# Kernel tuning notes

Hardware: AMD Instinct MI355X
Metric: run time of the kernel (lower is better)

## Reference

```python
import jax, jax.numpy as jnp
import numpy as np

EPS = 1e-5

def grid_sample_bilinear(img, grid):
    """torch F.grid_sample, mode='bilinear', padding_mode='zeros', align_corners=True.
    img: (b, c, H, W); grid: (b, Hg, Wg, 2) with (x, y) in [-1, 1]. Returns (b, c, Hg, Wg)."""
    H, W = img.shape[2], img.shape[3]
    x = (grid[..., 0] + 1.0) * 0.5 * (W - 1)
    y = (grid[..., 1] + 1.0) * 0.5 * (H - 1)
    x0 = jnp.floor(x); y0 = jnp.floor(y)
    x1 = x0 + 1.0;     y1 = y0 + 1.0
    wx1 = x - x0; wx0 = 1.0 - wx1
    wy1 = y - y0; wy0 = 1.0 - wy1

    def sample_one(img_b, yi, xi):
        # img_b: (c,H,W); yi, xi: (Hg,Wg) float corner coords
        valid = ((yi >= 0) & (yi < H) & (xi >= 0) & (xi < W)).astype(img_b.dtype)
        yc = jnp.clip(yi, 0, H - 1).astype(jnp.int32)
        xc = jnp.clip(xi, 0, W - 1).astype(jnp.int32)
        return img_b[:, yc, xc] * valid[None]  # (c,Hg,Wg)

    def per_batch(img_b, x0b, x1b, y0b, y1b, wx0b, wx1b, wy0b, wy1b):
        v = (sample_one(img_b, y0b, x0b) * (wy0b * wx0b)[None]
             + sample_one(img_b, y0b, x1b) * (wy0b * wx1b)[None]
             + sample_one(img_b, y1b, x0b) * (wy1b * wx0b)[None]
             + sample_one(img_b, y1b, x1b) * (wy1b * wx1b)[None])
        return v

    return jax.vmap(per_batch)(img, x0, x1, y0, y1, wx0, wx1, wy0, wy1)


def conv_bn_relu(x, w, gamma, beta):
    # 1x1 conv (no bias) + BatchNorm2d (batch stats, training-mode forward) + ReLU
    y = jnp.einsum('nchw,oc->nohw', x, w)
    mean = y.mean(axis=(0, 2, 3), keepdims=True)
    var = y.var(axis=(0, 2, 3), keepdims=True)
    y = (y - mean) * jax.lax.rsqrt(var + EPS)
    y = y * gamma[None, :, None, None] + beta[None, :, None, None]
    return jax.nn.relu(y)


def setup_inputs() -> dict:
    key = jax.random.key(0)
    ks = jax.random.split(key, 10)
    b, c, h, w, r = 1, 128, 64, 128, 4
    d = 2 * r + 1
    f1 = jax.random.normal(ks[0], (b, c, h, w), dtype=jnp.float32)
    f2 = jax.random.normal(ks[1], (b, c, h, w), dtype=jnp.float32)
    # coords: base pixel grid (x, y) plus a small random flow perturbation
    gy, gx = jnp.meshgrid(jnp.arange(h, dtype=jnp.float32), jnp.arange(w, dtype=jnp.float32), indexing='ij')
    base = jnp.stack([gx, gy], axis=0)[None]  # (1,2,h,w)
    coords = base + 2.0 * jax.random.normal(ks[2], (b, 2, h, w), dtype=jnp.float32)
    c1, c2, c3 = 96, 128, 64
    w1 = jax.random.normal(ks[3], (c1, 2 * c), dtype=jnp.float32) * 0.05
    w2 = jax.random.normal(ks[4], (c2, c1), dtype=jnp.float32) * 0.05
    w3 = jax.random.normal(ks[5], (c3, c2), dtype=jnp.float32) * 0.05
    w4 = jax.random.normal(ks[6], (1, c3), dtype=jnp.float32) * 0.05
    b4 = jnp.zeros((1,), dtype=jnp.float32)
    g1 = jnp.ones((c1,), jnp.float32); be1 = jnp.zeros((c1,), jnp.float32)
    g2 = jnp.ones((c2,), jnp.float32); be2 = jnp.zeros((c2,), jnp.float32)
    g3 = jnp.ones((c3,), jnp.float32); be3 = jnp.zeros((c3,), jnp.float32)
    # DAP: identity init + small noise so gradients are non-trivial
    wdap = jnp.eye(d * d, dtype=jnp.float32) + 0.01 * jax.random.normal(ks[7], (d * d, d * d), dtype=jnp.float32)
    return {"f1": f1, "f2": f2, "coords": coords,
            "w1": w1, "g1": g1, "be1": be1,
            "w2": w2, "g2": g2, "be2": be2,
            "w3": w3, "g3": g3, "be3": be3,
            "w4": w4, "b4": b4, "wdap": wdap, "radius": 4}


def reference(f1, f2, coords, w1, g1, be1, w2, g2, be2, w3, g3, be3, w4, b4, wdap, radius):
    b, c, h, w = f1.shape
    r = radius
    d = 2 * r + 1
    dx = jnp.linspace(-r, r, d, dtype=f1.dtype)
    delta = jnp.stack(jnp.meshgrid(dx, dx, indexing='ij'), axis=-1)  # (d,d,2)
    coords_p = jnp.transpose(coords, (0, 2, 3, 1))  # (b,h,w,2)
    cent = coords_p[:, None, :, None, :, :] + delta.reshape(1, d, 1, d, 1, 2)  # (b,d,h,d,w,2)
    cx = 2.0 * cent[..., 0] / (w - 1) - 1.0
    cy = 2.0 * cent[..., 1] / (h - 1) - 1.0
    grid = jnp.stack([cx, cy], axis=-1).reshape(b, d * h, d * w, 2)
    f2s = grid_sample_bilinear(f2, grid)                     # (b,c,d*h,d*w)
    f2s = f2s.reshape(b, c, d, h, d, w).transpose(0, 2, 4, 1, 3, 5)  # (b,d,d,c,h,w)
    f1e = jnp.broadcast_to(f1[:, None, None], (b, d, d, c, h, w))
    corr = jnp.concatenate([f1e, f2s], axis=3).reshape(b * d * d, 2 * c, h, w)
    x = conv_bn_relu(corr, w1, g1, be1)
    x = conv_bn_relu(x, w2, g2, be2)
    x = conv_bn_relu(x, w3, g3, be3)
    cost = jnp.einsum('nchw,oc->nohw', x, w4) + b4[None, :, None, None]  # (b*d*d,1,h,w)
    cost = cost.reshape(b, d * d, h, w)
    # DAP: 1x1 conv over the d*d displacement channels, no bias
    cost = jnp.einsum('bkhw,lk->blhw', cost, wdap)
    return cost  # (b, (2r+1)^2, h, w)
```

## Files before the change

### kernel.cpp

```cpp
#include <hip/hip_runtime.h>
#include <hip/hip_bf16.h>

#define H 64
#define W 128
#define P 8192
#define DD 81
#define NS 663552
#define C1 96
#define C2 128
#define C3 64
#define EPSF 1e-5f
#define NSLOT 128

#define X1S 104
#define X2S 136
#define X1TS 136

#define NGB 324
#define NGSLOT 8

typedef __attribute__((ext_vector_type(8))) short bf16x8;
typedef __attribute__((ext_vector_type(4))) float f32x4;

#define S1SUM 0
#define S1SSQ (S1SUM + NSLOT * C1)
#define M1SUM (S1SSQ + NSLOT * C1)
#define S3SUM (M1SUM + NSLOT * C1)
#define S3SSQ (S3SUM + NSLOT * C3)
#define GSLOT (S3SSQ + NSLOT * C3)
#define STATS_ZERO_FLOATS (GSLOT + NGSLOT * 9216)
#define S1Sc 126976
#define S1Tc (S1Sc + C1)
#define S2Sc (S1Tc + C1)
#define S2Tc (S2Sc + C2)
#define S3Sc (S2Tc + C2)
#define S3Tc (S3Sc + C3)
#define GOFF 127552
#define COST_OFF (GOFF + 9216)
#define FLOAT_END (COST_OFF + NS)
#define A_BYTE   ((size_t)FLOAT_END * 4)
#define G_BYTE   (A_BYTE + (size_t)P * 96 * 2)
#define W2BF_BYTE (G_BYTE + (size_t)P * 96 * 2)
#define W3BF_BYTE (W2BF_BYTE + (size_t)C2 * C1 * 2)
#define Y1_BYTE  (W3BF_BYTE + (size_t)C3 * C2 * 2)
#define Y3_BYTE  (Y1_BYTE + (size_t)NS * C1 * 2)
#define WS_NEEDED (Y3_BYTE + (size_t)NS * C3 * 2)

__device__ __forceinline__ float bflo(unsigned u) { return __uint_as_float(u << 16); }
__device__ __forceinline__ float bfhi(unsigned u) { return __uint_as_float(u & 0xffff0000u); }
__device__ __forceinline__ float bfu(unsigned short v) { return __uint_as_float((unsigned)v << 16); }

__device__ __forceinline__ unsigned pkbf(float a, float b) {
  __hip_bfloat162 h = __float22bfloat162_rn(make_float2(a, b));
  unsigned u; __builtin_memcpy(&u, &h, 4);
  return u;
}

__global__ __launch_bounds__(256) void k_prep(const float* __restrict__ f1,
                                              const float* __restrict__ f2,
                                              const float* __restrict__ w1,
                                              unsigned short* __restrict__ aT,
                                              unsigned short* __restrict__ gT) {
  __shared__ float tile[128][64];
  int t = threadIdx.x;
  int p0 = blockIdx.x * 64;
  int px = t & 63, q = t >> 6;
  int c0 = q * 24;
  for (int pass = 0; pass < 2; ++pass) {
    const float* src = pass ? f2 : f1;
    unsigned short* dst = pass ? gT : aT;
    int koff = pass ? 128 : 0;
    __syncthreads();
    for (int idx = t; idx < 8192; idx += 256) {
      int kk = idx >> 6, xx = idx & 63;
      tile[kk][xx] = src[kk * P + p0 + xx];
    }
    __syncthreads();
    float acc[24];
#pragma unroll
    for (int i = 0; i < 24; ++i) acc[i] = 0.f;
    for (int kk = 0; kk < 128; ++kk) {
      float fv = tile[kk][px];
#pragma unroll
      for (int i = 0; i < 24; ++i)
        acc[i] += w1[(c0 + i) * 256 + koff + kk] * fv;
    }
#pragma unroll
    for (int i = 0; i < 24; i += 4) {
      uint2 pk;
      pk.x = pkbf(acc[i + 0], acc[i + 1]);
      pk.y = pkbf(acc[i + 2], acc[i + 3]);
      *(uint2*)(dst + ((size_t)((c0 + i) >> 2) * P + p0 + px) * 4) = pk;
    }
  }
}

__global__ void k_wprep(const float* __restrict__ w2, const float* __restrict__ w3,
                        unsigned short* __restrict__ w2bf, unsigned short* __restrict__ w3bf) {
  int idx = blockIdx.x * 256 + threadIdx.x;
  if (idx < C2 * C1) {
    w2bf[idx] = (unsigned short)(pkbf(w2[idx], 0.f) & 0xffffu);
  } else if (idx < C2 * C1 + C3 * C2) {
    w3bf[idx - C2 * C1] = (unsigned short)(pkbf(w3[idx - C2 * C1], 0.f) & 0xffffu);
  }
}

__global__ __launch_bounds__(256) void k_sample(const float* __restrict__ coords,
                                                float* __restrict__ ws,
                                                const unsigned short* __restrict__ aT,
                                                const unsigned short* __restrict__ gT,
                                                unsigned short* __restrict__ y1T) {
  int t = threadIdx.x, b = blockIdx.x;
  int sub = b % 12;
  int ptile = b / 12;
  int cg = sub >> 1, jh = sub & 1;
  int j0 = jh * 5;
  int nj = 5 - jh;
  int c = cg * 4 + (t >> 6);
  int px = t & 63;
  int p = ptile * 64 + px;
  float cx = coords[p], cy = coords[P + p];
  float fx0 = floorf(cx), fy0 = floorf(cy);
  float wx1 = cx - fx0, wx0 = 1.f - wx1;
  float wy1 = cy - fy0, wy0 = 1.f - wy1;
  int ixb = (int)fx0 - 4 + j0, iyb = (int)fy0 - 4;
  int colOff[6];
  float vxv[6];
#pragma unroll
  for (int j = 0; j < 6; ++j) {
    int ix = ixb + j;
    vxv[j] = (ix >= 0 && ix < W) ? 1.f : 0.f;
    colOff[j] = min(max(ix, 0), W - 1);
  }
  float ewx0[5], ewx1[5];
#pragma unroll
  for (int j = 0; j < 5; ++j) { ewx0[j] = wx0 * vxv[j]; ewx1[j] = wx1 * vxv[j + 1]; }
  float av[4];
  {
    uint2 a2 = *(const uint2*)(aT + ((size_t)c * P + p) * 4);
    av[0] = bflo(a2.x); av[1] = bfhi(a2.x); av[2] = bflo(a2.y); av[3] = bfhi(a2.y);
  }
  const unsigned short* gc = gT + (size_t)c * P * 4;
  unsigned short* yb = y1T + ((size_t)c * P + p) * 4;
  float Hb[2][5][4];
  float sum[4] = {0.f, 0.f, 0.f, 0.f}, ssq[4] = {0.f, 0.f, 0.f, 0.f};
  float vyPrev = 0.f;
#pragma unroll
  for (int dy = 0; dy < 10; ++dy) {
    const int cur = dy & 1, prv = cur ^ 1;
    int iy = iyb + dy;
    float vy = (iy >= 0 && iy < H) ? 1.f : 0.f;
    const unsigned short* grow = gc + (size_t)(min(max(iy, 0), H - 1) * W) * 4;
    uint2 gv[6];
#pragma unroll
    for (int j = 0; j < 6; ++j) gv[j] = *(const uint2*)(grow + colOff[j] * 4);
#pragma unroll
    for (int j = 0; j < 5; ++j) {
      Hb[cur][j][0] = fmaf(ewx1[j], bflo(gv[j + 1].x), ewx0[j] * bflo(gv[j].x));
      Hb[cur][j][1] = fmaf(ewx1[j], bfhi(gv[j + 1].x), ewx0[j] * bfhi(gv[j].x));
      Hb[cur][j][2] = fmaf(ewx1[j], bflo(gv[j + 1].y), ewx0[j] * bflo(gv[j].y));
      Hb[cur][j][3] = fmaf(ewx1[j], bfhi(gv[j + 1].y), ewx0[j] * bfhi(gv[j].y));
    }
    if (dy >= 1) {
      const int dyk = dy - 1;
      float e0 = wy0 * vyPrev, e1 = wy1 * vy;
#pragma unroll
      for (int j = 0; j < 5; ++j) {
        if (j < nj) {
          float o0 = fmaf(e0, Hb[prv][j][0], fmaf(e1, Hb[cur][j][0], av[0]));
          float o1 = fmaf(e0, Hb[prv][j][1], fmaf(e1, Hb[cur][j][1], av[1]));
          float o2 = fmaf(e0, Hb[prv][j][2], fmaf(e1, Hb[cur][j][2], av[2]));
          float o3 = fmaf(e0, Hb[prv][j][3], fmaf(e1, Hb[cur][j][3], av[3]));
          sum[0] += o0; ssq[0] = fmaf(o0, o0, ssq[0]);
          sum[1] += o1; ssq[1] = fmaf(o1, o1, ssq[1]);
          sum[2] += o2; ssq[2] = fmaf(o2, o2, ssq[2]);
          sum[3] += o3; ssq[3] = fmaf(o3, o3, ssq[3]);
          uint2 pk;
          pk.x = pkbf(o0, o1);
          pk.y = pkbf(o2, o3);
          int kk = (j0 + j) * 9 + dyk;
          *(uint2*)(yb + (size_t)kk * 24 * P * 4) = pk;
        }
      }
    }
    vyPrev = vy;
  }
#pragma unroll
  for (int m = 1; m < 64; m <<= 1) {
#pragma unroll
    for (int e = 0; e < 4; ++e) {
      sum[e] += __shfl_xor(sum[e], m);
      ssq[e] += __shfl_xor(ssq[e], m);
    }
  }
  if ((t & 63) == 0) {
    int slot = b & (NSLOT - 1);
#pragma unroll
    for (int e = 0; e < 4; ++e) {
      atomicAdd(&ws[S1SUM + slot * C1 + c * 4 + e], sum[e]);
      atomicAdd(&ws[S1SSQ + slot * C1 + c * 4 + e], ssq[e]);
    }
  }
}

__global__ void k_finalize(float* __restrict__ ws, int sumO, int ssqO,
                           const float* __restrict__ gamma, const float* __restrict__ beta,
                           int sO, int tO, int C) {
  int c = threadIdx.x;
  if (c < C) {
    float su = 0.f, sq = 0.f;
    for (int s = 0; s < NSLOT; ++s) { su += ws[sumO + s * C + c]; sq += ws[ssqO + s * C + c]; }
    float mean = su * (1.0f / (float)NS);
    float var = sq * (1.0f / (float)NS) - mean * mean;
    float sc = gamma[c] * rsqrtf(var + EPSF);
    ws[sO + c] = sc;
    ws[tO + c] = beta[c] - mean * sc;
  }
}

__global__ __launch_bounds__(256) void k_gram(const unsigned short* __restrict__ y1T,
                                              float* __restrict__ ws) {
  __shared__ unsigned short x1t[96 * X1TS];
  int t = threadIdx.x, b = blockIdx.x;
  int w = t >> 6, l = t & 63;
  int lr = l & 15, lh = l >> 4;
  int i0 = (w >> 1) * 48, j0 = (w & 1) * 48;
  f32x4 acc[9];
  f32x4 zero4 = {0.f, 0.f, 0.f, 0.f};
#pragma unroll
  for (int q = 0; q < 9; ++q) acc[q] = zero4;
  int c = t >> 3, pg = t & 7;
  float s1v[4], t1v[4];
  if (c < 24) {
#pragma unroll
    for (int e = 0; e < 4; ++e) { s1v[e] = ws[S1Sc + c * 4 + e]; t1v[e] = ws[S1Tc + c * 4 + e]; }
  }
  float msum[4] = {0.f, 0.f, 0.f, 0.f};
  for (int it = 0; it < 16; ++it) {
    int idx = b * 16 + it;
    int k = idx >> 6, p0 = (idx & 63) << 7;
    const unsigned short* y1k = y1T + (size_t)k * P * 96;
    __syncthreads();
    if (c < 24) {
      int pbase = p0 + pg * 16;
      unsigned rowu[4][8];
#pragma unroll
      for (int ii = 0; ii < 8; ++ii) {
        uint4 v = *(const uint4*)(y1k + ((size_t)c * P + pbase + ii * 2) * 4);
        float x00 = fmaxf(0.f, fmaf(s1v[0], bflo(v.x), t1v[0]));
        float x10 = fmaxf(0.f, fmaf(s1v[1], bfhi(v.x), t1v[1]));
        float x20 = fmaxf(0.f, fmaf(s1v[2], bflo(v.y), t1v[2]));
        float x30 = fmaxf(0.f, fmaf(s1v[3], bfhi(v.y), t1v[3]));
        float x01 = fmaxf(0.f, fmaf(s1v[0], bflo(v.z), t1v[0]));
        float x11 = fmaxf(0.f, fmaf(s1v[1], bfhi(v.z), t1v[1]));
        float x21 = fmaxf(0.f, fmaf(s1v[2], bflo(v.w), t1v[2]));
        float x31 = fmaxf(0.f, fmaf(s1v[3], bfhi(v.w), t1v[3]));
        msum[0] += x00 + x01; msum[1] += x10 + x11;
        msum[2] += x20 + x21; msum[3] += x30 + x31;
        rowu[0][ii] = pkbf(x00, x01);
        rowu[1][ii] = pkbf(x10, x11);
        rowu[2][ii] = pkbf(x20, x21);
        rowu[3][ii] = pkbf(x30, x31);
      }
#pragma unroll
      for (int e = 0; e < 4; ++e) {
        unsigned short* dst = x1t + (c * 4 + e) * X1TS + pg * 16;
        uint4 pk0; pk0.x = rowu[e][0]; pk0.y = rowu[e][1]; pk0.z = rowu[e][2]; pk0.w = rowu[e][3];
        uint4 pk1; pk1.x = rowu[e][4]; pk1.y = rowu[e][5]; pk1.z = rowu[e][6]; pk1.w = rowu[e][7];
        *(uint4*)dst = pk0;
        *(uint4*)(dst + 8) = pk1;
      }
    }
    __syncthreads();
#pragma unroll
    for (int kk = 0; kk < 4; ++kk) {
      bf16x8 a3[3], b3[3];
#pragma unroll
      for (int a = 0; a < 3; ++a)
        a3[a] = *(const bf16x8*)(const void*)(x1t + (i0 + a * 16 + lr) * X1TS + kk * 32 + lh * 8);
#pragma unroll
      for (int bb = 0; bb < 3; ++bb)
        b3[bb] = *(const bf16x8*)(const void*)(x1t + (j0 + bb * 16 + lr) * X1TS + kk * 32 + lh * 8);
#pragma unroll
      for (int a = 0; a < 3; ++a)
#pragma unroll
        for (int bb = 0; bb < 3; ++bb)
          acc[a * 3 + bb] = __builtin_amdgcn_mfma_f32_16x16x32_bf16(a3[a], b3[bb], acc[a * 3 + bb], 0, 0, 0);
    }
  }
  {
    float* gp = ws + GSLOT + (b & (NGSLOT - 1)) * 9216;
#pragma unroll
    for (int a = 0; a < 3; ++a)
#pragma unroll
      for (int bb = 0; bb < 3; ++bb) {
        int ti = (w >> 1) * 3 + a, tj = (w & 1) * 3 + bb;
        f32x4 v = acc[a * 3 + bb];
#pragma unroll
        for (int r = 0; r < 4; ++r)
          atomicAdd(&gp[(ti * 16 + lh * 4 + r) * 96 + tj * 16 + lr], v[r]);
      }
  }
  if (c < 24) {
#pragma unroll
    for (int m = 1; m < 8; m <<= 1)
#pragma unroll
      for (int e = 0; e < 4; ++e) msum[e] += __shfl_xor(msum[e], m);
    if (pg == 0) {
      int slot = b & (NSLOT - 1);
#pragma unroll
      for (int e = 0; e < 4; ++e) atomicAdd(&ws[M1SUM + slot * C1 + c * 4 + e], msum[e]);
    }
  }
}

__global__ void k_greduce(float* __restrict__ ws) {
  int e = blockIdx.x * 256 + threadIdx.x;
  float s = 0.f;
#pragma unroll
  for (int g = 0; g < NGSLOT; ++g) s += ws[GSLOT + g * 9216 + e];
  ws[GOFF + e] = s;
}

__global__ __launch_bounds__(256) void k_fin2g(float* __restrict__ ws,
                                               const unsigned short* __restrict__ w2bf,
                                               const float* __restrict__ g2,
                                               const float* __restrict__ be2) {
  __shared__ float wrow[96];
  __shared__ float m1f[96];
  __shared__ float red[8];
  int o = blockIdx.x, t = threadIdx.x;
  if (t < 96) {
    wrow[t] = bfu(w2bf[o * 96 + t]);
    float s = 0.f;
    for (int sl = 0; sl < NSLOT; ++sl) s += ws[M1SUM + sl * C1 + t];
    m1f[t] = s;
  }
  __syncthreads();
  float quad = 0.f;
  for (int e = t; e < 9216; e += 256) {
    int i = e / 96, j = e - i * 96;
    quad = fmaf(wrow[i] * wrow[j], ws[GOFF + e], quad);
  }
  float msm = (t < 96) ? wrow[t] * m1f[t] : 0.f;
#pragma unroll
  for (int m = 1; m < 64; m <<= 1) { quad += __shfl_xor(quad, m); msm += __shfl_xor(msm, m); }
  if ((t & 63) == 0) { red[t >> 6] = quad; red[4 + (t >> 6)] = msm; }
  __syncthreads();
  if (t == 0) {
    float q = red[0] + red[1] + red[2] + red[3];
    float mm = red[4] + red[5] + red[6] + red[7];
    float mean = mm * (1.0f / (float)NS);
    float var = q * (1.0f / (float)NS) - mean * mean;
    float sc = g2[o] * rsqrtf(var + EPSF);
    ws[S2Sc + o] = sc;
    ws[S2Tc + o] = be2[o] - mean * sc;
  }
}

__device__ __forceinline__ void build_x1(const unsigned short* __restrict__ y1k,
                                         const float* __restrict__ ws,
                                         unsigned short* lds, int p0, int t) {
  int s = t >> 1, hh = t & 1;
  int p = p0 + s;
  const float* s1p = ws + S1Sc;
  const float* t1p = ws + S1Tc;
  unsigned short* base = lds + s * X1S + hh * 48;
#pragma unroll
  for (int i2 = 0; i2 < 6; ++i2) {
    int c0 = hh * 12 + i2 * 2;
    uint2 va = *(const uint2*)(y1k + ((size_t)c0 * P + p) * 4);
    uint2 vb = *(const uint2*)(y1k + ((size_t)(c0 + 1) * P + p) * 4);
    int cb = c0 * 4;
    float x0 = fmaxf(0.f, fmaf(s1p[cb + 0], bflo(va.x), t1p[cb + 0]));
    float x1 = fmaxf(0.f, fmaf(s1p[cb + 1], bfhi(va.x), t1p[cb + 1]));
    float x2 = fmaxf(0.f, fmaf(s1p[cb + 2], bflo(va.y), t1p[cb + 2]));
    float x3 = fmaxf(0.f, fmaf(s1p[cb + 3], bfhi(va.y), t1p[cb + 3]));
    float x4 = fmaxf(0.f, fmaf(s1p[cb + 4], bflo(vb.x), t1p[cb + 4]));
    float x5 = fmaxf(0.f, fmaf(s1p[cb + 5], bfhi(vb.x), t1p[cb + 5]));
    float x6 = fmaxf(0.f, fmaf(s1p[cb + 6], bflo(vb.y), t1p[cb + 6]));
    float x7 = fmaxf(0.f, fmaf(s1p[cb + 7], bfhi(vb.y), t1p[cb + 7]));
    uint4 pk;
    pk.x = pkbf(x0, x1); pk.y = pkbf(x2, x3); pk.z = pkbf(x4, x5); pk.w = pkbf(x6, x7);
    *(uint4*)(base + i2 * 8) = pk;
  }
}

__global__ __launch_bounds__(256) void k_l23(const unsigned short* __restrict__ y1T,
                                             float* __restrict__ ws,
                                             const unsigned short* __restrict__ w2bf,
                                             const unsigned short* __restrict__ w3bf,
                                             unsigned short* __restrict__ y3T) {
  __shared__ unsigned short ldss[128 * X1S];
  int t = threadIdx.x, b = blockIdx.x;
  int k = b >> 6, p0 = (b & 63) << 7;
  size_t n0 = (size_t)k * P + p0;
  int slot = b & (NSLOT - 1);
  const unsigned short* y1k = y1T + (size_t)k * P * 96;
  build_x1(y1k, ws, ldss, p0, t);
  __syncthreads();
  int l = t & 63, wv = t >> 6;
  int o0w = wv * 32;
  int lr = l & 15, lh = l >> 4;
  bf16x8 af[2][3];
#pragma unroll
  for (int m = 0; m < 2; ++m)
#pragma unroll
    for (int kk = 0; kk < 3; ++kk)
      af[m][kk] = *(const bf16x8*)(const void*)(w2bf + (size_t)(o0w + m * 16 + lr) * 96 + kk * 32 + lh * 8);
  f32x4 acc[2][8];
  f32x4 zero4 = {0.f, 0.f, 0.f, 0.f};
#pragma unroll
  for (int m = 0; m < 2; ++m)
#pragma unroll
    for (int n = 0; n < 8; ++n) acc[m][n] = zero4;
#pragma unroll
  for (int kk = 0; kk < 3; ++kk)
#pragma unroll
    for (int n = 0; n < 8; ++n) {
      bf16x8 bfr = *(const bf16x8*)(const void*)(ldss + (n * 16 + lr) * X1S + kk * 32 + lh * 8);
      acc[0][n] = __builtin_amdgcn_mfma_f32_16x16x32_bf16(af[0][kk], bfr, acc[0][n], 0, 0, 0);
      acc[1][n] = __builtin_amdgcn_mfma_f32_16x16x32_bf16(af[1][kk], bfr, acc[1][n], 0, 0, 0);
    }
  float s2v[2][4], t2v[2][4];
#pragma unroll
  for (int m = 0; m < 2; ++m)
#pragma unroll
    for (int r = 0; r < 4; ++r) {
      int cc = o0w + m * 16 + lh * 4 + r;
      s2v[m][r] = ws[S2Sc + cc];
      t2v[m][r] = ws[S2Tc + cc];
    }
  int o2 = wv * 16;
  int ch4 = wv * 4 + lh;
  bf16x8 af2[4];
#pragma unroll
  for (int kk = 0; kk < 4; ++kk)
    af2[kk] = *(const bf16x8*)(const void*)(w3bf + (size_t)(o2 + lr) * 128 + kk * 32 + lh * 8);
  unsigned short* x2s = ldss;
  float ssum[4] = {0.f, 0.f, 0.f, 0.f}, sssq[4] = {0.f, 0.f, 0.f, 0.f};
#pragma unroll
  for (int h = 0; h < 2; ++h) {
    __syncthreads();
#pragma unroll
    for (int m = 0; m < 2; ++m)
#pragma unroll
      for (int n2 = 0; n2 < 4; ++n2) {
        f32x4 v = acc[m][h * 4 + n2];
        float x0 = fmaxf(0.f, fmaf(s2v[m][0], v[0], t2v[m][0]));
        float x1v = fmaxf(0.f, fmaf(s2v[m][1], v[1], t2v[m][1]));
        float x2v = fmaxf(0.f, fmaf(s2v[m][2], v[2], t2v[m][2]));
        float x3 = fmaxf(0.f, fmaf(s2v[m][3], v[3], t2v[m][3]));
        uint2 pk;
        pk.x = pkbf(x0, x1v);
        pk.y = pkbf(x2v, x3);
        *(uint2*)(x2s + (n2 * 16 + lr) * X2S + o0w + m * 16 + lh * 4) = pk;
      }
    __syncthreads();
    f32x4 acc2[4];
#pragma unroll
    for (int n2 = 0; n2 < 4; ++n2) acc2[n2] = zero4;
#pragma unroll
    for (int kk = 0; kk < 4; ++kk)
#pragma unroll
      for (int n2 = 0; n2 < 4; ++n2) {
        bf16x8 bfr = *(const bf16x8*)(const void*)(x2s + (n2 * 16 + lr) * X2S + kk * 32 + lh * 8);
        acc2[n2] = __builtin_amdgcn_mfma_f32_16x16x32_bf16(af2[kk], bfr, acc2[n2], 0, 0, 0);
      }
#pragma unroll
    for (int n2 = 0; n2 < 4; ++n2) {
      f32x4 v = acc2[n2];
#pragma unroll
      for (int r = 0; r < 4; ++r) { float x = v[r]; ssum[r] += x; sssq[r] = fmaf(x, x, sssq[r]); }
      uint2 pk;
      pk.x = pkbf(v[0], v[1]);
      pk.y = pkbf(v[2], v[3]);
      size_t n = n0 + h * 64 + n2 * 16 + lr;
      *(uint2*)(y3T + ((size_t)ch4 * NS + n) * 4) = pk;
    }
  }
#pragma unroll
  for (int msk = 1; msk < 16; msk <<= 1)
#pragma unroll
    for (int i = 0; i < 4; ++i) { ssum[i] += __shfl_xor(ssum[i], msk); sssq[i] += __shfl_xor(sssq[i], msk); }
  if (lr == 0) {
#pragma unroll
    for (int r = 0; r < 4; ++r) {
      int o = o2 + lh * 4 + r;
      atomicAdd(&ws[S3SUM + slot * C3 + o], ssum[r]);
      atomicAdd(&ws[S3SSQ + slot * C3 + o], sssq[r]);
    }
  }
}

__global__ __launch_bounds__(256) void k_layer4(const unsigned short* __restrict__ y3T,
                                                float* __restrict__ ws,
                                                const float* __restrict__ w4,
                                                const float* __restrict__ b4) {
  size_t n = (size_t)blockIdx.x * 256 + threadIdx.x;
  const float* s3p = ws + S3Sc;
  const float* t3p = ws + S3Tc;
  float acc = 0.f;
#pragma unroll
  for (int c16 = 0; c16 < 16; ++c16) {
    uint2 v = *(const uint2*)(y3T + ((size_t)c16 * NS + n) * 4);
    int c = c16 * 4;
    acc += fmaxf(0.f, fmaf(s3p[c + 0], bflo(v.x), t3p[c + 0])) * w4[c + 0];
    acc += fmaxf(0.f, fmaf(s3p[c + 1], bfhi(v.x), t3p[c + 1])) * w4[c + 1];
    acc += fmaxf(0.f, fmaf(s3p[c + 2], bflo(v.y), t3p[c + 2])) * w4[c + 2];
    acc += fmaxf(0.f, fmaf(s3p[c + 3], bfhi(v.y), t3p[c + 3])) * w4[c + 3];
  }
  ws[COST_OFF + n] = acc + b4[0];
}

__global__ __launch_bounds__(256) void k_dap(const float* __restrict__ ws,
                                             const float* __restrict__ wdap,
                                             float* __restrict__ out) {
  __shared__ float wd[DD * DD];
  int t = threadIdx.x;
  for (int i = t; i < DD * DD; i += 256) wd[i] = wdap[i];
  __syncthreads();
  int p = blockIdx.x * 32 + (t & 31);
  int lg = t >> 5;
  const float* cost = ws + COST_OFF;
  float cr[81];
#pragma unroll
  for (int kk = 0; kk < 81; ++kk) cr[kk] = cost[kk * P + p];
  for (int l = lg; l < 81; l += 8) {
    float acc = 0.f;
#pragma unroll
    for (int kk = 0; kk < 81; ++kk) acc = fmaf(wd[l * 81 + kk], cr[kk], acc);
    out[(size_t)l * P + p] = acc;
  }
}

__global__ void k_marker(float* out) { out[0] = 1.0e30f; }

extern "C" void kernel_launch(void* const* d_in, const int* in_sizes, int n_in,
                              void* d_out, int out_size, void* d_ws, size_t ws_size,
                              hipStream_t stream) {
  const float* f1 = (const float*)d_in[0];
  const float* f2 = (const float*)d_in[1];
  const float* coords = (const float*)d_in[2];
  const float* w1 = (const float*)d_in[3];
  const float* g1 = (const float*)d_in[4];
  const float* be1 = (const float*)d_in[5];
  const float* w2 = (const float*)d_in[6];
  const float* g2 = (const float*)d_in[7];
  const float* be2 = (const float*)d_in[8];
  const float* w3 = (const float*)d_in[9];
  const float* g3 = (const float*)d_in[10];
  const float* be3 = (const float*)d_in[11];
  const float* w4 = (const float*)d_in[12];
  const float* b4 = (const float*)d_in[13];
  const float* wdap = (const float*)d_in[14];
  float* out = (float*)d_out;
  float* ws = (float*)d_ws;

  if (ws_size < WS_NEEDED) {
    k_marker<<<1, 1, 0, stream>>>(out);
    return;
  }
  unsigned short* aT = (unsigned short*)((char*)d_ws + A_BYTE);
  unsigned short* gT = (unsigned short*)((char*)d_ws + G_BYTE);
  unsigned short* w2bf = (unsigned short*)((char*)d_ws + W2BF_BYTE);
  unsigned short* w3bf = (unsigned short*)((char*)d_ws + W3BF_BYTE);
  unsigned short* y1T = (unsigned short*)((char*)d_ws + Y1_BYTE);
  unsigned short* y3T = (unsigned short*)((char*)d_ws + Y3_BYTE);

  hipMemsetAsync(d_ws, 0, (size_t)STATS_ZERO_FLOATS * 4, stream);
  k_prep<<<128, 256, 0, stream>>>(f1, f2, w1, aT, gT);
  k_wprep<<<80, 256, 0, stream>>>(w2, w3, w2bf, w3bf);
  k_sample<<<1536, 256, 0, stream>>>(coords, ws, aT, gT, y1T);
  k_finalize<<<1, 128, 0, stream>>>(ws, S1SUM, S1SSQ, g1, be1, S1Sc, S1Tc, C1);
  k_gram<<<NGB, 256, 0, stream>>>(y1T, ws);
  k_greduce<<<36, 256, 0, stream>>>(ws);
  k_fin2g<<<128, 256, 0, stream>>>(ws, w2bf, g2, be2);
  k_l23<<<5184, 256, 0, stream>>>(y1T, ws, w2bf, w3bf, y3T);
  k_finalize<<<1, 128, 0, stream>>>(ws, S3SUM, S3SSQ, g3, be3, S3Sc, S3Tc, C3);
  k_layer4<<<2592, 256, 0, stream>>>(y3T, ws, w4, b4);
  k_dap<<<256, 256, 0, stream>>>(ws, wdap, out);
}
```

Baseline: 284.9 us.

## Fuse layer-4 projection into DAP kernel and halve l23 tile per block

Merges the layer-4 1x1 conv (BN+ReLU+dot with w4) into the DAP kernel, so per-pixel cost values stay in shared memory instead of being written to and re-read from a global cost buffer, and one launch is removed. The l23 kernel now handles 64 pixels per block instead of 128 and launches twice as many blocks. That uses fewer accumulator registers and less LDS per block, which can raise occupancy, but the weight fragments are loaded more often. The fused kernel runs on only 256 blocks, so the layer-4 pass over y3T is spread across fewer blocks than before, which risks reduced parallelism.

```diff
diff --git a/kernel.cpp b/kernel.cpp
--- a/kernel.cpp
+++ b/kernel.cpp
@@ -36,8 +36,7 @@
 #define S3Sc (S2Tc + C2)
 #define S3Tc (S3Sc + C3)
 #define GOFF 127552
-#define COST_OFF (GOFF + 9216)
-#define FLOAT_END (COST_OFF + NS)
+#define FLOAT_END (GOFF + 9216)
 #define A_BYTE   ((size_t)FLOAT_END * 4)
 #define G_BYTE   (A_BYTE + (size_t)P * 96 * 2)
 #define W2BF_BYTE (G_BYTE + (size_t)P * 96 * 2)
@@ -358,46 +357,36 @@
   }
 }
 
-__device__ __forceinline__ void build_x1(const unsigned short* __restrict__ y1k,
-                                         const float* __restrict__ ws,
-                                         unsigned short* lds, int p0, int t) {
-  int s = t >> 1, hh = t & 1;
-  int p = p0 + s;
-  const float* s1p = ws + S1Sc;
-  const float* t1p = ws + S1Tc;
-  unsigned short* base = lds + s * X1S + hh * 48;
-#pragma unroll
-  for (int i2 = 0; i2 < 6; ++i2) {
-    int c0 = hh * 12 + i2 * 2;
-    uint2 va = *(const uint2*)(y1k + ((size_t)c0 * P + p) * 4);
-    uint2 vb = *(const uint2*)(y1k + ((size_t)(c0 + 1) * P + p) * 4);
-    int cb = c0 * 4;
-    float x0 = fmaxf(0.f, fmaf(s1p[cb + 0], bflo(va.x), t1p[cb + 0]));
-    float x1 = fmaxf(0.f, fmaf(s1p[cb + 1], bfhi(va.x), t1p[cb + 1]));
-    float x2 = fmaxf(0.f, fmaf(s1p[cb + 2], bflo(va.y), t1p[cb + 2]));
-    float x3 = fmaxf(0.f, fmaf(s1p[cb + 3], bfhi(va.y), t1p[cb + 3]));
-    float x4 = fmaxf(0.f, fmaf(s1p[cb + 4], bflo(vb.x), t1p[cb + 4]));
-    float x5 = fmaxf(0.f, fmaf(s1p[cb + 5], bfhi(vb.x), t1p[cb + 5]));
-    float x6 = fmaxf(0.f, fmaf(s1p[cb + 6], bflo(vb.y), t1p[cb + 6]));
-    float x7 = fmaxf(0.f, fmaf(s1p[cb + 7], bfhi(vb.y), t1p[cb + 7]));
-    uint4 pk;
-    pk.x = pkbf(x0, x1); pk.y = pkbf(x2, x3); pk.z = pkbf(x4, x5); pk.w = pkbf(x6, x7);
-    *(uint4*)(base + i2 * 8) = pk;
-  }
-}
-
 __global__ __launch_bounds__(256) void k_l23(const unsigned short* __restrict__ y1T,
                                              float* __restrict__ ws,
                                              const unsigned short* __restrict__ w2bf,
                                              const unsigned short* __restrict__ w3bf,
                                              unsigned short* __restrict__ y3T) {
-  __shared__ unsigned short ldss[128 * X1S];
+  __shared__ unsigned short ldss[64 * X2S];
   int t = threadIdx.x, b = blockIdx.x;
-  int k = b >> 6, p0 = (b & 63) << 7;
+  int k = b >> 7, p0 = (b & 127) << 6;
   size_t n0 = (size_t)k * P + p0;
   int slot = b & (NSLOT - 1);
   const unsigned short* y1k = y1T + (size_t)k * P * 96;
-  build_x1(y1k, ws, ldss, p0, t);
+  {
+    int s = t >> 2, q = t & 3;
+    int p = p0 + s;
+    const float* s1p = ws + S1Sc;
+    const float* t1p = ws + S1Tc;
+    unsigned short* base = ldss + s * X1S + q * 24;
+#pragma unroll
+    for (int i = 0; i < 6; ++i) {
+      int c4i = q * 6 + i;
+      uint2 v = *(const uint2*)(y1k + ((size_t)c4i * P + p) * 4);
+      int cb = c4i * 4;
+      float x0 = fmaxf(0.f, fmaf(s1p[cb + 0], bflo(v.x), t1p[cb + 0]));
+      float x1 = fmaxf(0.f, fmaf(s1p[cb + 1], bfhi(v.x), t1p[cb + 1]));
+      float x2 = fmaxf(0.f, fmaf(s1p[cb + 2], bflo(v.y), t1p[cb + 2]));
+      float x3 = fmaxf(0.f, fmaf(s1p[cb + 3], bfhi(v.y), t1p[cb + 3]));
+      uint2 pk; pk.x = pkbf(x0, x1); pk.y = pkbf(x2, x3);
+      *(uint2*)(base + i * 4) = pk;
+    }
+  }
   __syncthreads();
   int l = t & 63, wv = t >> 6;
   int o0w = wv * 32;
@@ -408,16 +397,16 @@
 #pragma unroll
     for (int kk = 0; kk < 3; ++kk)
       af[m][kk] = *(const bf16x8*)(const void*)(w2bf + (size_t)(o0w + m * 16 + lr) * 96 + kk * 32 + lh * 8);
-  f32x4 acc[2][8];
+  f32x4 acc[2][4];
   f32x4 zero4 = {0.f, 0.f, 0.f, 0.f};
 #pragma unroll
   for (int m = 0; m < 2; ++m)
 #pragma unroll
-    for (int n = 0; n < 8; ++n) acc[m][n] = zero4;
+    for (int n = 0; n < 4; ++n) acc[m][n] = zero4;
 #pragma unroll
   for (int kk = 0; kk < 3; ++kk)
 #pragma unroll
-    for (int n = 0; n < 8; ++n) {
+    for (int n = 0; n < 4; ++n) {
       bf16x8 bfr = *(const bf16x8*)(const void*)(ldss + (n * 16 + lr) * X1S + kk * 32 + lh * 8);
       acc[0][n] = __builtin_amdgcn_mfma_f32_16x16x32_bf16(af[0][kk], bfr, acc[0][n], 0, 0, 0);
       acc[1][n] = __builtin_amdgcn_mfma_f32_16x16x32_bf16(af[1][kk], bfr, acc[1][n], 0, 0, 0);
@@ -437,47 +426,43 @@
 #pragma unroll
   for (int kk = 0; kk < 4; ++kk)
     af2[kk] = *(const bf16x8*)(const void*)(w3bf + (size_t)(o2 + lr) * 128 + kk * 32 + lh * 8);
-  unsigned short* x2s = ldss;
+  __syncthreads();
+#pragma unroll
+  for (int m = 0; m < 2; ++m)
+#pragma unroll
+    for (int n2 = 0; n2 < 4; ++n2) {
+      f32x4 v = acc[m][n2];
+      float x0 = fmaxf(0.f, fmaf(s2v[m][0], v[0], t2v[m][0]));
+      float x1v = fmaxf(0.f, fmaf(s2v[m][1], v[1], t2v[m][1]));
+      float x2v = fmaxf(0.f, fmaf(s2v[m][2], v[2], t2v[m][2]));
+      float x3 = fmaxf(0.f, fmaf(s2v[m][3], v[3], t2v[m][3]));
+      uint2 pk;
+      pk.x = pkbf(x0, x1v);
+      pk.y = pkbf(x2v, x3);
+      *(uint2*)(ldss + (n2 * 16 + lr) * X2S + o0w + m * 16 + lh * 4) = pk;
+    }
+  __syncthreads();
+  f32x4 acc2[4];
+#pragma unroll
+  for (int n2 = 0; n2 < 4; ++n2) acc2[n2] = zero4;
+#pragma unroll
+  for (int kk = 0; kk < 4; ++kk)
+#pragma unroll
+    for (int n2 = 0; n2 < 4; ++n2) {
+      bf16x8 bfr = *(const bf16x8*)(const void*)(ldss + (n2 * 16 + lr) * X2S + kk * 32 + lh * 8);
+      acc2[n2] = __builtin_amdgcn_mfma_f32_16x16x32_bf16(af2[kk], bfr, acc2[n2], 0, 0, 0);
+    }
   float ssum[4] = {0.f, 0.f, 0.f, 0.f}, sssq[4] = {0.f, 0.f, 0.f, 0.f};
 #pragma unroll
-  for (int h = 0; h < 2; ++h) {
-    __syncthreads();
-#pragma unroll
-    for (int m = 0; m < 2; ++m)
-#pragma unroll
-      for (int n2 = 0; n2 < 4; ++n2) {
-        f32x4 v = acc[m][h * 4 + n2];
-        float x0 = fmaxf(0.f, fmaf(s2v[m][0], v[0], t2v[m][0]));
-        float x1v = fmaxf(0.f, fmaf(s2v[m][1], v[1], t2v[m][1]));
-        float x2v = fmaxf(0.f, fmaf(s2v[m][2], v[2], t2v[m][2]));
-        float x3 = fmaxf(0.f, fmaf(s2v[m][3], v[3], t2v[m][3]));
-        uint2 pk;
-        pk.x = pkbf(x0, x1v);
-        pk.y = pkbf(x2v, x3);
-        *(uint2*)(x2s + (n2 * 16 + lr) * X2S + o0w + m * 16 + lh * 4) = pk;
-      }
-    __syncthreads();
-    f32x4 acc2[4];
-#pragma unroll
-    for (int n2 = 0; n2 < 4; ++n2) acc2[n2] = zero4;
-#pragma unroll
-    for (int kk = 0; kk < 4; ++kk)
-#pragma unroll
-      for (int n2 = 0; n2 < 4; ++n2) {
-        bf16x8 bfr = *(const bf16x8*)(const void*)(x2s + (n2 * 16 + lr) * X2S + kk * 32 + lh * 8);
-        acc2[n2] = __builtin_amdgcn_mfma_f32_16x16x32_bf16(af2[kk], bfr, acc2[n2], 0, 0, 0);
-      }
-#pragma unroll
-    for (int n2 = 0; n2 < 4; ++n2) {
-      f32x4 v = acc2[n2];
-#pragma unroll
-      for (int r = 0; r < 4; ++r) { float x = v[r]; ssum[r] += x; sssq[r] = fmaf(x, x, sssq[r]); }
-      uint2 pk;
-      pk.x = pkbf(v[0], v[1]);
-      pk.y = pkbf(v[2], v[3]);
-      size_t n = n0 + h * 64 + n2 * 16 + lr;
-      *(uint2*)(y3T + ((size_t)ch4 * NS + n) * 4) = pk;
-    }
+  for (int n2 = 0; n2 < 4; ++n2) {
+    f32x4 v = acc2[n2];
+#pragma unroll
+    for (int r = 0; r < 4; ++r) { float x = v[r]; ssum[r] += x; sssq[r] = fmaf(x, x, sssq[r]); }
+    uint2 pk;
+    pk.x = pkbf(v[0], v[1]);
+    pk.y = pkbf(v[2], v[3]);
+    size_t n = n0 + n2 * 16 + lr;
+    *(uint2*)(y3T + ((size_t)ch4 * NS + n) * 4) = pk;
   }
 #pragma unroll
   for (int msk = 1; msk < 16; msk <<= 1)
@@ -493,44 +478,49 @@
   }
 }
 
-__global__ __launch_bounds__(256) void k_layer4(const unsigned short* __restrict__ y3T,
-                                                float* __restrict__ ws,
-                                                const float* __restrict__ w4,
-                                                const float* __restrict__ b4) {
-  size_t n = (size_t)blockIdx.x * 256 + threadIdx.x;
-  const float* s3p = ws + S3Sc;
-  const float* t3p = ws + S3Tc;
-  float acc = 0.f;
-#pragma unroll
-  for (int c16 = 0; c16 < 16; ++c16) {
-    uint2 v = *(const uint2*)(y3T + ((size_t)c16 * NS + n) * 4);
-    int c = c16 * 4;
-    acc += fmaxf(0.f, fmaf(s3p[c + 0], bflo(v.x), t3p[c + 0])) * w4[c + 0];
-    acc += fmaxf(0.f, fmaf(s3p[c + 1], bfhi(v.x), t3p[c + 1])) * w4[c + 1];
-    acc += fmaxf(0.f, fmaf(s3p[c + 2], bflo(v.y), t3p[c + 2])) * w4[c + 2];
-    acc += fmaxf(0.f, fmaf(s3p[c + 3], bfhi(v.y), t3p[c + 3])) * w4[c + 3];
-  }
-  ws[COST_OFF + n] = acc + b4[0];
-}
-
-__global__ __launch_bounds__(256) void k_dap(const float* __restrict__ ws,
-                                             const float* __restrict__ wdap,
-                                             float* __restrict__ out) {
+__global__ __launch_bounds__(256) void k_dap4(const unsigned short* __restrict__ y3T,
+                                              const float* __restrict__ ws,
+                                              const float* __restrict__ w4,
+                                              const float* __restrict__ b4,
+                                              const float* __restrict__ wdap,
+                                              float* __restrict__ out) {
   __shared__ float wd[DD * DD];
+  __shared__ float cs[DD][33];
+  __shared__ float coef[3][64];
   int t = threadIdx.x;
+  int p0 = blockIdx.x * 32;
   for (int i = t; i < DD * DD; i += 256) wd[i] = wdap[i];
-  __syncthreads();
-  int p = blockIdx.x * 32 + (t & 31);
-  int lg = t >> 5;
-  const float* cost = ws + COST_OFF;
-  float cr[81];
-#pragma unroll
-  for (int kk = 0; kk < 81; ++kk) cr[kk] = cost[kk * P + p];
-  for (int l = lg; l < 81; l += 8) {
+  if (t < 64) {
+    coef[0][t] = ws[S3Sc + t];
+    coef[1][t] = ws[S3Tc + t];
+    coef[2][t] = w4[t];
+  }
+  __syncthreads();
+  float b4v = b4[0];
+  int px = t & 31, kg = t >> 5;
+  for (int k = kg; k < DD; k += 8) {
+    size_t n = (size_t)k * P + p0 + px;
     float acc = 0.f;
 #pragma unroll
-    for (int kk = 0; kk < 81; ++kk) acc = fmaf(wd[l * 81 + kk], cr[kk], acc);
-    out[(size_t)l * P + p] = acc;
+    for (int c16 = 0; c16 < 16; ++c16) {
+      uint2 v = *(const uint2*)(y3T + ((size_t)c16 * NS + n) * 4);
+      int c = c16 * 4;
+      acc += fmaxf(0.f, fmaf(coef[0][c + 0], bflo(v.x), coef[1][c + 0])) * coef[2][c + 0];
+      acc += fmaxf(0.f, fmaf(coef[0][c + 1], bfhi(v.x), coef[1][c + 1])) * coef[2][c + 1];
+      acc += fmaxf(0.f, fmaf(coef[0][c + 2], bflo(v.y), coef[1][c + 2])) * coef[2][c + 2];
+      acc += fmaxf(0.f, fmaf(coef[0][c + 3], bfhi(v.y), coef[1][c + 3])) * coef[2][c + 3];
+    }
+    cs[k][px] = acc + b4v;
+  }
+  __syncthreads();
+  float cr[DD];
+#pragma unroll
+  for (int kk = 0; kk < DD; ++kk) cr[kk] = cs[kk][px];
+  for (int l = kg; l < DD; l += 8) {
+    float acc = 0.f;
+#pragma unroll
+    for (int kk = 0; kk < DD; ++kk) acc = fmaf(wd[l * 81 + kk], cr[kk], acc);
+    out[(size_t)l * P + p0 + px] = acc;
   }
 }
 
@@ -576,8 +566,7 @@
   k_gram<<<NGB, 256, 0, stream>>>(y1T, ws);
   k_greduce<<<36, 256, 0, stream>>>(ws);
   k_fin2g<<<128, 256, 0, stream>>>(ws, w2bf, g2, be2);
-  k_l23<<<5184, 256, 0, stream>>>(y1T, ws, w2bf, w3bf, y3T);
+  k_l23<<<10368, 256, 0, stream>>>(y1T, ws, w2bf, w3bf, y3T);
   k_finalize<<<1, 128, 0, stream>>>(ws, S3SUM, S3SSQ, g3, be3, S3Sc, S3Tc, C3);
-  k_layer4<<<2592, 256, 0, stream>>>(y3T, ws, w4, b4);
-  k_dap<<<256, 256, 0, stream>>>(ws, wdap, out);
-}
+  k_dap4<<<256, 256, 0, stream>>>(y3T, ws, w4, b4, wdap, out);
+}
```

Result: slower. 348.7 us (+22.4%).
